# Kernel optimization log

Measured on AMD Instinct MI355X. Metric: run time of the kernel, lower is better.

The kernel has to match this reference:

```python
import jax, jax.numpy as jnp
import numpy as np

B, T, D, H = 2, 2048, 2048, 32
HD = D // H
# quantization scales (constructor-time attributes in the original repo)
A_PROJ = 3e-4   # q/k/v proj alpha (W8A8B8O8Linear)
A_QK = 2e-5     # qk_bmm alpha (BMM_S8T_S8N_F32T)
A_PV = 1e-2     # pv_bmm alpha (BMM_S8T_S8N_S8T)
A_OUT = 1e-4    # out_proj alpha (W8A8BFP32OFP32Linear)


def _i8(key, shape):
    return jax.random.randint(key, shape, -128, 128, dtype=jnp.int32).astype(jnp.int8)


def setup_inputs() -> dict:
    key = jax.random.key(0)
    ks = jax.random.split(key, 10)
    hidden_states = _i8(ks[0], (B, T, D))
    # causal mask, 0 on/below diagonal, large negative above
    causal = jnp.triu(jnp.full((T, T), -1e9, dtype=jnp.float32), k=1)
    attention_mask = jnp.broadcast_to(causal, (B, 1, T, T))
    return {
        "hidden_states": hidden_states,
        "attention_mask": attention_mask,
        "Wq": _i8(ks[1], (D, D)), "bq": _i8(ks[2], (D,)),
        "Wk": _i8(ks[3], (D, D)), "bk": _i8(ks[4], (D,)),
        "Wv": _i8(ks[5], (D, D)), "bv": _i8(ks[6], (D,)),
        "Wo": _i8(ks[7], (D, D)),
        "bo": jax.random.normal(ks[8], (D,), dtype=jnp.float32),
    }


def _w8a8b8o8(x_i8, W_i8, b_i8, alpha):
    # int8 GEMM -> int32 accum; epilogue: alpha*acc + bias, saturate to int8
    acc = jnp.einsum('btk,nk->btn', x_i8.astype(jnp.int32), W_i8.astype(jnp.int32))
    y = alpha * acc.astype(jnp.float32) + b_i8.astype(jnp.float32)
    return jnp.clip(jnp.round(y), -128, 127).astype(jnp.int8)


def reference(hidden_states, attention_mask, Wq, bq, Wk, bk, Wv, bv, Wo, bo):
    # q/k/v projections: int8 in, int8 out
    q = _w8a8b8o8(hidden_states, Wq, bq, A_PROJ)
    k = _w8a8b8o8(hidden_states, Wk, bk, A_PROJ)
    v = _w8a8b8o8(hidden_states, Wv, bv, A_PROJ)

    def shape(x):  # [B,T,D] -> [B,H,T,HD]
        return x.reshape(B, T, H, HD).transpose(0, 2, 1, 3)

    qh, kh, vh = shape(q), shape(k), shape(v)

    # qk_bmm (BMM_S8T_S8N_F32T): fp32 = alpha * int8 q @ k^T
    attn = A_QK * jnp.einsum('bhtd,bhsd->bhts',
                             qh.astype(jnp.int32), kh.astype(jnp.int32)).astype(jnp.float32)
    attn = attn + attention_mask  # [B,1,T,T] broadcasts over heads
    attn = jnp.maximum(attn, jnp.finfo(jnp.float32).min)
    probs = jax.nn.softmax(attn, axis=-1)

    # quantize probs: p.mul_(127).round_() -> int8
    p_i8 = jnp.clip(jnp.round(probs * 127.0), -128, 127).astype(jnp.int8)

    # pv_bmm (BMM_S8T_S8N_S8T): int8 out = sat(round(alpha * p @ v))
    pv = jnp.einsum('bhts,bhsd->bhtd', p_i8.astype(jnp.int32), vh.astype(jnp.int32))
    attn_out_i8 = jnp.clip(jnp.round(A_PV * pv.astype(jnp.float32)), -128, 127).astype(jnp.int8)

    # [B,H,T,HD] -> [B,T,D]
    attn_out = attn_out_i8.transpose(0, 2, 1, 3).reshape(B, T, D)

    # out_proj (W8A8BFP32OFP32Linear): fp32 = alpha*(x@W^T) + fp32 bias
    acc = jnp.einsum('btk,nk->btn', attn_out.astype(jnp.int32), Wo.astype(jnp.int32))
    out = A_OUT * acc.astype(jnp.float32) + bo
    return out
```

## Files before the change

### kernel.cpp

```cpp
#include <hip/hip_runtime.h>
#include <cstdint>

#define A_PROJ 3e-4f
#define A_QK   2e-5f
#define A_PV   1e-2f
#define A_OUT  1e-4f

#define NB 2
#define NT 2048
#define ND 2048
#define NH 32
#define NHD 64
#define NM (NB*NT)

typedef int v4i __attribute__((ext_vector_type(4)));

__device__ __forceinline__ int8_t sat8(float y) {
  float r = rintf(y);
  r = fminf(fmaxf(r, -128.f), 127.f);
  return (int8_t)(int)r;
}

__device__ __forceinline__ float exp2_fast(float x) {
  return __builtin_amdgcn_exp2f(x);
}

__device__ __forceinline__ void gl2lds16(const int8_t* g, int8_t* l) {
  __builtin_amdgcn_global_load_lds(
      (const __attribute__((address_space(1))) void*)g,
      (__attribute__((address_space(3))) void*)l, 16, 0, 0);
}

__device__ __forceinline__ uint32_t pack_lo4(float f0, float f1, float f2, float f3) {
  uint32_t u0 = __float_as_uint(f0), u1 = __float_as_uint(f1);
  uint32_t u2 = __float_as_uint(f2), u3 = __float_as_uint(f3);
  uint32_t lo = __builtin_amdgcn_perm(u1, u0, 0x04000400u);
  uint32_t hi = __builtin_amdgcn_perm(u3, u2, 0x04000400u);
  return __builtin_amdgcn_perm(hi, lo, 0x05040100u);
}

#define NWW (ND*ND/4)
__global__ void pack_all(const int* __restrict__ X,
                         const int* __restrict__ W0, const int* __restrict__ W1,
                         const int* __restrict__ W2, const int* __restrict__ W3,
                         int8_t* __restrict__ dX, int8_t* __restrict__ dW0,
                         int8_t* __restrict__ dW1, int8_t* __restrict__ dW2,
                         int8_t* __restrict__ dW3) {
  int i = blockIdx.x * blockDim.x + threadIdx.x;
  const int nx = NM*ND/4;
  const int* src; int8_t* dst; int off;
  if (i < nx) { src = X; dst = dX; off = i; }
  else {
    int j = i - nx;
    int r = j >> 20;
    off = j & (NWW - 1);
    src = (r == 0) ? W0 : (r == 1) ? W1 : (r == 2) ? W2 : W3;
    dst = (r == 0) ? dW0 : (r == 1) ? dW1 : (r == 2) ? dW2 : dW3;
  }
  int4 v = ((const int4*)src)[off];
  uint32_t p = (uint32_t)(v.x & 255) | ((uint32_t)(v.y & 255) << 8) |
               ((uint32_t)(v.z & 255) << 16) | ((uint32_t)(v.w & 255) << 24);
  ((uint32_t*)dst)[off] = p;
}

__global__ __launch_bounds__(256) void gemm_qkv(
    const int8_t* __restrict__ X,
    const int8_t* __restrict__ Wq, const int8_t* __restrict__ Wk, const int8_t* __restrict__ Wv,
    const int* __restrict__ bq, const int* __restrict__ bk, const int* __restrict__ bv,
    int8_t* __restrict__ Qh, int8_t* __restrict__ Kh, int8_t* __restrict__ Vt)
{
  __shared__ __align__(16) int8_t As[2][128][64];
  __shared__ __align__(16) int8_t Bs[2][128][64];
  const int z = blockIdx.z;
  const int8_t* W  = (z == 0) ? Wq : ((z == 1) ? Wk : Wv);
  const int* bias  = (z == 0) ? bq : ((z == 1) ? bk : bv);
  const int m0 = blockIdx.x * 128, n0 = blockIdx.y * 128;
  const int tid = threadIdx.x, lane = tid & 63, wave = tid >> 6;
  const int wm = wave >> 1, wn = wave & 1;
  const int l15 = lane & 15, quad = lane >> 4;

  const int srow = lane >> 2;
  const int scol = (((lane & 3) ^ ((lane >> 3) & 3)) * 16);
  const int rqcol = (quad ^ ((l15 >> 1) & 3)) * 16;

  v4i acc[4][4];
  const v4i vzero = {0, 0, 0, 0};
  #pragma unroll
  for (int i = 0; i < 4; ++i)
    #pragma unroll
    for (int j = 0; j < 4; ++j) acc[i][j] = vzero;

  for (int k0 = 0; k0 < ND; k0 += 128) {
    #pragma unroll
    for (int j = 0; j < 8; ++j) {
      int slot = j * 4 + wave;
      int sl = slot & 15;
      int hh = sl >> 3, rblk = sl & 7;
      int row = rblk * 16 + srow;
      if (slot < 16) {
        gl2lds16(&X[(size_t)(m0 + row) * ND + k0 + hh * 64 + scol], &As[hh][rblk * 16][0]);
      } else {
        gl2lds16(&W[(size_t)(n0 + row) * ND + k0 + hh * 64 + scol], &Bs[hh][rblk * 16][0]);
      }
    }
    __syncthreads();
    #pragma unroll
    for (int hh = 0; hh < 2; ++hh) {
      v4i a[4], b[4];
      #pragma unroll
      for (int mt = 0; mt < 4; ++mt) a[mt] = *(const v4i*)&As[hh][wm*64 + mt*16 + l15][rqcol];
      #pragma unroll
      for (int nt = 0; nt < 4; ++nt) b[nt] = *(const v4i*)&Bs[hh][wn*64 + nt*16 + l15][rqcol];
      #pragma unroll
      for (int mt = 0; mt < 4; ++mt)
        #pragma unroll
        for (int nt = 0; nt < 4; ++nt)
          acc[mt][nt] = __builtin_amdgcn_mfma_i32_16x16x64_i8(a[mt], b[nt], acc[mt][nt], 0, 0, 0);
    }
    __syncthreads();
  }

  float bf[4];
  #pragma unroll
  for (int nt = 0; nt < 4; ++nt) bf[nt] = (float)bias[n0 + wn*64 + nt*16 + l15];

  if (z == 2) {
    #pragma unroll
    for (int mt = 0; mt < 4; ++mt)
      #pragma unroll
      for (int nt = 0; nt < 4; ++nt) {
        int tbase = (m0 + wm*64 + mt*16 + quad*4) & (NT - 1);
        int bb = (m0 + wm*64) >> 11;
        int n = n0 + wn*64 + nt*16 + l15;
        int hh = n >> 6, hd = n & (NHD - 1);
        uint32_t pk = 0;
        #pragma unroll
        for (int r = 0; r < 4; ++r) {
          uint32_t q = (uint32_t)(uint8_t)sat8(A_PROJ * (float)acc[mt][nt][r] + bf[nt]);
          pk |= q << (8 * r);
        }
        size_t bh = (size_t)bb * NH + hh;
        *(uint32_t*)&Vt[(bh * NHD + hd) * NT + tbase] = pk;
      }
  } else {
    int8_t* O = (z == 0) ? Qh : Kh;
    #pragma unroll
    for (int mt = 0; mt < 4; ++mt)
      #pragma unroll
      for (int nt = 0; nt < 4; ++nt)
        #pragma unroll
        for (int r = 0; r < 4; ++r) {
          int m = m0 + wm*64 + mt*16 + quad*4 + r;
          int n = n0 + wn*64 + nt*16 + l15;
          int8_t q = sat8(A_PROJ * (float)acc[mt][nt][r] + bf[nt]);
          int bb = m >> 11, t = m & (NT - 1);
          int hh = n >> 6, hd = n & (NHD - 1);
          size_t bh = (size_t)bb * NH + hh;
          O[(bh * NT + t) * NHD + hd] = q;
        }
  }
}

__global__ __launch_bounds__(512, 8) void attn_fused(
    const int8_t* __restrict__ Qh, const int8_t* __restrict__ Kh, const int8_t* __restrict__ Vt,
    int8_t* __restrict__ AO)
{
  __shared__ __align__(16) int8_t Ksd[2][64][64];
  __shared__ __align__(16) int8_t Vsd[2][64][64];
  __shared__ __align__(16) uint32_t Ps32[8][16][20];

  const int bx = blockIdx.x;
  const int bh = blockIdx.y;
  const int tid = threadIdx.x, lane = tid & 63, wave = tid >> 6;
  const int l15 = lane & 15, quad = lane >> 4;
  const v4i vzero = {0, 0, 0, 0};
  const float MAGIC = 12582912.0f;
  const float C2 = 2.8853900817779268e-05f;

  const int jg = bh >> 4;
  const int x = (jg == 0) ? bx : (jg == 1) ? (15 - bx)
              : (jg == 2) ? ((bx + 8) & 15) : ((7 - bx) & 15);

  const int8_t* Qp = Qh + (size_t)bh * NT * NHD;
  const int8_t* Kp = Kh + (size_t)bh * NT * NHD;
  const int8_t* Vp = Vt + (size_t)bh * NHD * NT;
  const int bb = bh >> 5, hhead = bh & (NH - 1);

  const int t0 = x * 128;
  const int nsteps = 2 * x + 2;
  const int tw = t0 + wave * 16;
  const int tme = tw + l15;

  const int strow = lane >> 2;
  const int stcol = (((lane & 3) ^ ((lane >> 3) & 3)) * 16);
  const int fcol  = (quad ^ ((l15 >> 1) & 3)) * 16;

  v4i qf = *(const v4i*)&Qp[(size_t)(tw + l15) * NHD + quad * 16];

  float ls0 = 0.f, ls1 = 0.f, ls2 = 0.f, ls3 = 0.f;
  if (wave < 4)
    gl2lds16(&Kp[(size_t)(0 + wave*16 + strow) * NHD + stcol], &Ksd[0][wave*16][0]);
  __syncthreads();
  int cur = 0;
  for (int st = 0; st < nsteps; ++st) {
    if (st + 1 < nsteps && wave < 4)
      gl2lds16(&Kp[(size_t)((st+1)*64 + wave*16 + strow) * NHD + stcol],
               &Ksd[cur ^ 1][wave*16][0]);
    const int s0 = st * 64;
    if (s0 <= tw + 15) {
      v4i kf[4];
      #pragma unroll
      for (int mt = 0; mt < 4; ++mt) kf[mt] = *(const v4i*)&Ksd[cur][mt*16 + l15][fcol];
      if (s0 + 63 <= tw) {
        #pragma unroll
        for (int mt = 0; mt < 4; ++mt) {
          v4i sa = __builtin_amdgcn_mfma_i32_16x16x64_i8(kf[mt], qf, vzero, 0, 0, 0);
          ls0 += exp2_fast(C2 * (float)sa[0]);
          ls1 += exp2_fast(C2 * (float)sa[1]);
          ls2 += exp2_fast(C2 * (float)sa[2]);
          ls3 += exp2_fast(C2 * (float)sa[3]);
        }
      } else {
        #pragma unroll
        for (int mt = 0; mt < 4; ++mt) {
          v4i sa = __builtin_amdgcn_mfma_i32_16x16x64_i8(kf[mt], qf, vzero, 0, 0, 0);
          const int sb = s0 + mt*16 + quad*4;
          ls0 += (sb + 0 <= tme) ? exp2_fast(C2 * (float)sa[0]) : 0.f;
          ls1 += (sb + 1 <= tme) ? exp2_fast(C2 * (float)sa[1]) : 0.f;
          ls2 += (sb + 2 <= tme) ? exp2_fast(C2 * (float)sa[2]) : 0.f;
          ls3 += (sb + 3 <= tme) ? exp2_fast(C2 * (float)sa[3]) : 0.f;
        }
      }
    }
    __syncthreads();
    cur ^= 1;
  }
  float lsum = (ls0 + ls1) + (ls2 + ls3);
  lsum += __shfl_xor(lsum, 16, 64);
  lsum += __shfl_xor(lsum, 32, 64);
  const float linv = 127.0f / lsum;

  v4i accv[4];
  #pragma unroll
  for (int jj = 0; jj < 4; ++jj) accv[jj] = vzero;

  if (wave < 4)
    gl2lds16(&Kp[(size_t)(0 + wave*16 + strow) * NHD + stcol], &Ksd[0][wave*16][0]);
  else
    gl2lds16(&Vp[(size_t)((wave-4)*16 + strow) * NT + 0 + stcol], &Vsd[0][(wave-4)*16][0]);
  __syncthreads();
  cur = 0;
  for (int st = 0; st < nsteps; ++st) {
    if (st + 1 < nsteps) {
      if (wave < 4)
        gl2lds16(&Kp[(size_t)((st+1)*64 + wave*16 + strow) * NHD + stcol],
                 &Ksd[cur ^ 1][wave*16][0]);
      else
        gl2lds16(&Vp[(size_t)((wave-4)*16 + strow) * NT + (st+1)*64 + stcol],
                 &Vsd[cur ^ 1][(wave-4)*16][0]);
    }
    const int s0 = st * 64;
    if (s0 <= tw + 15) {
      v4i kf[4];
      #pragma unroll
      for (int mt = 0; mt < 4; ++mt) kf[mt] = *(const v4i*)&Ksd[cur][mt*16 + l15][fcol];
      if (s0 + 63 <= tw) {
        #pragma unroll
        for (int mt = 0; mt < 4; ++mt) {
          v4i sa = __builtin_amdgcn_mfma_i32_16x16x64_i8(kf[mt], qf, vzero, 0, 0, 0);
          float f0 = fmaf(exp2_fast(C2 * (float)sa[0]), linv, MAGIC);
          float f1 = fmaf(exp2_fast(C2 * (float)sa[1]), linv, MAGIC);
          float f2 = fmaf(exp2_fast(C2 * (float)sa[2]), linv, MAGIC);
          float f3 = fmaf(exp2_fast(C2 * (float)sa[3]), linv, MAGIC);
          Ps32[wave][l15][mt*4 + quad] = pack_lo4(f0, f1, f2, f3);
        }
      } else {
        #pragma unroll
        for (int mt = 0; mt < 4; ++mt) {
          v4i sa = __builtin_amdgcn_mfma_i32_16x16x64_i8(kf[mt], qf, vzero, 0, 0, 0);
          const int sb = s0 + mt*16 + quad*4;
          float e0 = (sb + 0 <= tme) ? exp2_fast(C2 * (float)sa[0]) : 0.f;
          float e1 = (sb + 1 <= tme) ? exp2_fast(C2 * (float)sa[1]) : 0.f;
          float e2 = (sb + 2 <= tme) ? exp2_fast(C2 * (float)sa[2]) : 0.f;
          float e3 = (sb + 3 <= tme) ? exp2_fast(C2 * (float)sa[3]) : 0.f;
          Ps32[wave][l15][mt*4 + quad] =
              pack_lo4(fmaf(e0, linv, MAGIC), fmaf(e1, linv, MAGIC),
                       fmaf(e2, linv, MAGIC), fmaf(e3, linv, MAGIC));
        }
      }
      v4i ap = *(const v4i*)&Ps32[wave][l15][quad*4];
      #pragma unroll
      for (int nt2 = 0; nt2 < 4; ++nt2) {
        v4i bvv = *(const v4i*)&Vsd[cur][nt2*16 + l15][fcol];
        accv[nt2] = __builtin_amdgcn_mfma_i32_16x16x64_i8(ap, bvv, accv[nt2], 0, 0, 0);
      }
    }
    __syncthreads();
    cur ^= 1;
  }

  #pragma unroll
  for (int nt2 = 0; nt2 < 4; ++nt2)
    #pragma unroll
    for (int r = 0; r < 4; ++r) {
      int t = tw + quad*4 + r;
      int d = nt2*16 + l15;
      AO[((size_t)bb * NT + t) * ND + hhead * NHD + d] = sat8(A_PV * (float)accv[nt2][r]);
    }
}

__global__ __launch_bounds__(256) void gemm_out(
    const int8_t* __restrict__ X, const int8_t* __restrict__ W,
    const float* __restrict__ bo, float* __restrict__ out)
{
  __shared__ __align__(16) int8_t As[2][128][64];
  __shared__ __align__(16) int8_t Bs[2][128][64];
  const int m0 = blockIdx.x * 128, n0 = blockIdx.y * 128;
  const int tid = threadIdx.x, lane = tid & 63, wave = tid >> 6;
  const int wm = wave >> 1, wn = wave & 1;
  const int l15 = lane & 15, quad = lane >> 4;
  const int srow = lane >> 2;
  const int scol = (((lane & 3) ^ ((lane >> 3) & 3)) * 16);
  const int rqcol = (quad ^ ((l15 >> 1) & 3)) * 16;

  v4i acc[4][4];
  const v4i vzero = {0, 0, 0, 0};
  #pragma unroll
  for (int i = 0; i < 4; ++i)
    #pragma unroll
    for (int j = 0; j < 4; ++j) acc[i][j] = vzero;

  for (int k0 = 0; k0 < ND; k0 += 128) {
    #pragma unroll
    for (int j = 0; j < 8; ++j) {
      int slot = j * 4 + wave;
      int sl = slot & 15;
      int hh = sl >> 3, rblk = sl & 7;
      int row = rblk * 16 + srow;
      if (slot < 16) {
        gl2lds16(&X[(size_t)(m0 + row) * ND + k0 + hh * 64 + scol], &As[hh][rblk * 16][0]);
      } else {
        gl2lds16(&W[(size_t)(n0 + row) * ND + k0 + hh * 64 + scol], &Bs[hh][rblk * 16][0]);
      }
    }
    __syncthreads();
    #pragma unroll
    for (int hh = 0; hh < 2; ++hh) {
      v4i a[4], b[4];
      #pragma unroll
      for (int mt = 0; mt < 4; ++mt) a[mt] = *(const v4i*)&As[hh][wm*64 + mt*16 + l15][rqcol];
      #pragma unroll
      for (int nt = 0; nt < 4; ++nt) b[nt] = *(const v4i*)&Bs[hh][wn*64 + nt*16 + l15][rqcol];
      #pragma unroll
      for (int mt = 0; mt < 4; ++mt)
        #pragma unroll
        for (int nt = 0; nt < 4; ++nt)
          acc[mt][nt] = __builtin_amdgcn_mfma_i32_16x16x64_i8(a[mt], b[nt], acc[mt][nt], 0, 0, 0);
    }
    __syncthreads();
  }

  float bf[4];
  #pragma unroll
  for (int nt = 0; nt < 4; ++nt) bf[nt] = bo[n0 + wn*64 + nt*16 + l15];

  #pragma unroll
  for (int mt = 0; mt < 4; ++mt)
    #pragma unroll
    for (int nt = 0; nt < 4; ++nt)
      #pragma unroll
      for (int r = 0; r < 4; ++r) {
        int m = m0 + wm*64 + mt*16 + quad*4 + r;
        int n = n0 + wn*64 + nt*16 + l15;
        out[(size_t)m * ND + n] = A_OUT * (float)acc[mt][nt][r] + bf[nt];
      }
}

extern "C" void kernel_launch(void* const* d_in, const int* in_sizes, int n_in,
                              void* d_out, int out_size, void* d_ws, size_t ws_size,
                              hipStream_t stream)
{
  const int*   hs  = (const int*)d_in[0];
  const int*   Wq  = (const int*)d_in[2];
  const int*   bq  = (const int*)d_in[3];
  const int*   Wk  = (const int*)d_in[4];
  const int*   bkb = (const int*)d_in[5];
  const int*   Wv  = (const int*)d_in[6];
  const int*   bvb = (const int*)d_in[7];
  const int*   Wo  = (const int*)d_in[8];
  const float* bo  = (const float*)d_in[9];
  float* out = (float*)d_out;

  char* ws = (char*)d_ws;
  const size_t SZ_X = (size_t)NM * ND;
  const size_t SZ_W = (size_t)ND * ND;
  const size_t SZ_H = (size_t)NB * NH * NT * NHD;
  int8_t* Xp  = (int8_t*)ws;
  int8_t* Wqp = (int8_t*)(ws + SZ_X);
  int8_t* Wkp = Wqp + SZ_W;
  int8_t* Wvp = Wkp + SZ_W;
  int8_t* Wop = Wvp + SZ_W;
  int8_t* Qh  = Wop + SZ_W;
  int8_t* Kh  = Qh + SZ_H;
  int8_t* Vt  = Kh + SZ_H;
  int8_t* AO  = Xp;

  const int ntot = (int)(SZ_X/4 + 4 * (SZ_W/4));
  pack_all<<<(ntot + 255) / 256, 256, 0, stream>>>(hs, Wq, Wk, Wv, Wo,
                                                   Xp, Wqp, Wkp, Wvp, Wop);

  gemm_qkv<<<dim3(NM/128, ND/128, 3), 256, 0, stream>>>(Xp, Wqp, Wkp, Wvp, bq, bkb, bvb, Qh, Kh, Vt);
  attn_fused<<<dim3(16, NB*NH), 512, 0, stream>>>(Qh, Kh, Vt, AO);
  gemm_out<<<dim3(NM/128, ND/128), 256, 0, stream>>>(AO, Wop, bo, out);
}
```

Baseline: 314.8 us.

## Double-buffer LDS tiles with prefetch in projection and output GEMMs

The QKV projection and output projection GEMMs now stream 64-wide K slices into alternating LDS buffers. The next slice is loaded while MFMAs run on the current one, so the main loop has one barrier per step instead of load-sync-compute-sync. Source and destination pointers are precomputed outside the loop to cut per-iteration address arithmetic. In exchange there are twice as many, smaller K iterations, and overlap depends on the barrier draining the async global-to-LDS copies.

After: 312.2 us. No clear change (-0.9%).

```diff
diff --git a/kernel.cpp b/kernel.cpp
--- a/kernel.cpp
+++ b/kernel.cpp
@@ -83,6 +83,17 @@
   const int scol = (((lane & 3) ^ ((lane >> 3) & 3)) * 16);
   const int rqcol = (quad ^ ((l15 >> 1) & 3)) * 16;
 
+  const int8_t* srcp[4];
+  int8_t* dstp[4];
+  #pragma unroll
+  for (int j = 0; j < 4; ++j) {
+    int slot = j * 4 + wave;
+    int rblk = slot & 7;
+    int row = rblk * 16 + srow;
+    if (slot < 8) { srcp[j] = &X[(size_t)(m0 + row) * ND + scol]; dstp[j] = &As[0][rblk*16][0]; }
+    else          { srcp[j] = &W[(size_t)(n0 + row) * ND + scol]; dstp[j] = &Bs[0][rblk*16][0]; }
+  }
+
   v4i acc[4][4];
   const v4i vzero = {0, 0, 0, 0};
   #pragma unroll
@@ -90,34 +101,29 @@
     #pragma unroll
     for (int j = 0; j < 4; ++j) acc[i][j] = vzero;
 
-  for (int k0 = 0; k0 < ND; k0 += 128) {
-    #pragma unroll
-    for (int j = 0; j < 8; ++j) {
-      int slot = j * 4 + wave;
-      int sl = slot & 15;
-      int hh = sl >> 3, rblk = sl & 7;
-      int row = rblk * 16 + srow;
-      if (slot < 16) {
-        gl2lds16(&X[(size_t)(m0 + row) * ND + k0 + hh * 64 + scol], &As[hh][rblk * 16][0]);
-      } else {
-        gl2lds16(&W[(size_t)(n0 + row) * ND + k0 + hh * 64 + scol], &Bs[hh][rblk * 16][0]);
-      }
-    }
+  #pragma unroll
+  for (int j = 0; j < 4; ++j) gl2lds16(srcp[j], dstp[j]);
+  __syncthreads();
+
+  int cur = 0;
+  for (int k0 = 64; k0 <= ND; k0 += 64) {
+    if (k0 < ND) {
+      const int boff = (cur ^ 1) * 128 * 64;
+      #pragma unroll
+      for (int j = 0; j < 4; ++j) gl2lds16(srcp[j] + k0, dstp[j] + boff);
+    }
+    v4i a[4], b[4];
+    #pragma unroll
+    for (int mt = 0; mt < 4; ++mt) a[mt] = *(const v4i*)&As[cur][wm*64 + mt*16 + l15][rqcol];
+    #pragma unroll
+    for (int nt = 0; nt < 4; ++nt) b[nt] = *(const v4i*)&Bs[cur][wn*64 + nt*16 + l15][rqcol];
+    #pragma unroll
+    for (int mt = 0; mt < 4; ++mt)
+      #pragma unroll
+      for (int nt = 0; nt < 4; ++nt)
+        acc[mt][nt] = __builtin_amdgcn_mfma_i32_16x16x64_i8(a[mt], b[nt], acc[mt][nt], 0, 0, 0);
     __syncthreads();
-    #pragma unroll
-    for (int hh = 0; hh < 2; ++hh) {
-      v4i a[4], b[4];
-      #pragma unroll
-      for (int mt = 0; mt < 4; ++mt) a[mt] = *(const v4i*)&As[hh][wm*64 + mt*16 + l15][rqcol];
-      #pragma unroll
-      for (int nt = 0; nt < 4; ++nt) b[nt] = *(const v4i*)&Bs[hh][wn*64 + nt*16 + l15][rqcol];
-      #pragma unroll
-      for (int mt = 0; mt < 4; ++mt)
-        #pragma unroll
-        for (int nt = 0; nt < 4; ++nt)
-          acc[mt][nt] = __builtin_amdgcn_mfma_i32_16x16x64_i8(a[mt], b[nt], acc[mt][nt], 0, 0, 0);
-    }
-    __syncthreads();
+    cur ^= 1;
   }
 
   float bf[4];
@@ -323,6 +329,17 @@
   const int scol = (((lane & 3) ^ ((lane >> 3) & 3)) * 16);
   const int rqcol = (quad ^ ((l15 >> 1) & 3)) * 16;
 
+  const int8_t* srcp[4];
+  int8_t* dstp[4];
+  #pragma unroll
+  for (int j = 0; j < 4; ++j) {
+    int slot = j * 4 + wave;
+    int rblk = slot & 7;
+    int row = rblk * 16 + srow;
+    if (slot < 8) { srcp[j] = &X[(size_t)(m0 + row) * ND + scol]; dstp[j] = &As[0][rblk*16][0]; }
+    else          { srcp[j] = &W[(size_t)(n0 + row) * ND + scol]; dstp[j] = &Bs[0][rblk*16][0]; }
+  }
+
   v4i acc[4][4];
   const v4i vzero = {0, 0, 0, 0};
   #pragma unroll
@@ -330,34 +347,29 @@
     #pragma unroll
     for (int j = 0; j < 4; ++j) acc[i][j] = vzero;
 
-  for (int k0 = 0; k0 < ND; k0 += 128) {
-    #pragma unroll
-    for (int j = 0; j < 8; ++j) {
-      int slot = j * 4 + wave;
-      int sl = slot & 15;
-      int hh = sl >> 3, rblk = sl & 7;
-      int row = rblk * 16 + srow;
-      if (slot < 16) {
-        gl2lds16(&X[(size_t)(m0 + row) * ND + k0 + hh * 64 + scol], &As[hh][rblk * 16][0]);
-      } else {
-        gl2lds16(&W[(size_t)(n0 + row) * ND + k0 + hh * 64 + scol], &Bs[hh][rblk * 16][0]);
-      }
-    }
+  #pragma unroll
+  for (int j = 0; j < 4; ++j) gl2lds16(srcp[j], dstp[j]);
+  __syncthreads();
+
+  int cur = 0;
+  for (int k0 = 64; k0 <= ND; k0 += 64) {
+    if (k0 < ND) {
+      const int boff = (cur ^ 1) * 128 * 64;
+      #pragma unroll
+      for (int j = 0; j < 4; ++j) gl2lds16(srcp[j] + k0, dstp[j] + boff);
+    }
+    v4i a[4], b[4];
+    #pragma unroll
+    for (int mt = 0; mt < 4; ++mt) a[mt] = *(const v4i*)&As[cur][wm*64 + mt*16 + l15][rqcol];
+    #pragma unroll
+    for (int nt = 0; nt < 4; ++nt) b[nt] = *(const v4i*)&Bs[cur][wn*64 + nt*16 + l15][rqcol];
+    #pragma unroll
+    for (int mt = 0; mt < 4; ++mt)
+      #pragma unroll
+      for (int nt = 0; nt < 4; ++nt)
+        acc[mt][nt] = __builtin_amdgcn_mfma_i32_16x16x64_i8(a[mt], b[nt], acc[mt][nt], 0, 0, 0);
     __syncthreads();
-    #pragma unroll
-    for (int hh = 0; hh < 2; ++hh) {
-      v4i a[4], b[4];
-      #pragma unroll
-      for (int mt = 0; mt < 4; ++mt) a[mt] = *(const v4i*)&As[hh][wm*64 + mt*16 + l15][rqcol];
-      #pragma unroll
-      for (int nt = 0; nt < 4; ++nt) b[nt] = *(const v4i*)&Bs[hh][wn*64 + nt*16 + l15][rqcol];
-      #pragma unroll
-      for (int mt = 0; mt < 4; ++mt)
-        #pragma unroll
-        for (int nt = 0; nt < 4; ++nt)
-          acc[mt][nt] = __builtin_amdgcn_mfma_i32_16x16x64_i8(a[mt], b[nt], acc[mt][nt], 0, 0, 0);
-    }
-    __syncthreads();
+    cur ^= 1;
   }
 
   float bf[4];
```
